# Performance work log

Measured on AMD Instinct MI355X. Metric: run time of the kernel, lower is better.

The kernel has to match this reference:

```python
import jax, jax.numpy as jnp
import numpy as np

D_MODEL, WIN, STRIDE, NHEAD, HEAD_DIM, FFN_H = 96, 16, 8, 6, 16, 192
INNER = NHEAD * HEAD_DIM
EPS = 1e-5


def _ln(x, g, b):
    m = jnp.mean(x, axis=-1, keepdims=True)
    v = jnp.mean((x - m) ** 2, axis=-1, keepdims=True)
    return (x - m) / jnp.sqrt(v + EPS) * g + b


def setup_inputs() -> dict:
    key = jax.random.key(0)
    ks = jax.random.split(key, 16)
    B, L, D = 32, 8192, D_MODEL
    sd = lambda n: 1.0 / np.sqrt(n)
    return {
        "x": jax.random.normal(ks[0], (B, L, D), jnp.float32),
        "ln1_g": jnp.ones((D,), jnp.float32),
        "ln1_b": jnp.zeros((D,), jnp.float32),
        "qkv_w": jax.random.normal(ks[1], (D, 3 * INNER), jnp.float32) * sd(D),
        "qkv_b": jnp.zeros((3 * INNER,), jnp.float32),
        "out_w": jax.random.normal(ks[2], (INNER, D), jnp.float32) * sd(INNER),
        "out_b": jnp.zeros((D,), jnp.float32),
        "ln2_g": jnp.ones((D,), jnp.float32),
        "ln2_b": jnp.zeros((D,), jnp.float32),
        "ffn_w1": jax.random.normal(ks[3], (D, FFN_H), jnp.float32) * sd(D),
        "ffn_b1": jnp.zeros((FFN_H,), jnp.float32),
        "ffn_w2": jax.random.normal(ks[4], (FFN_H, D), jnp.float32) * sd(FFN_H),
        "ffn_b2": jnp.zeros((D,), jnp.float32),
        "pln_g": jnp.ones((D,), jnp.float32),
        "pln_b": jnp.zeros((D,), jnp.float32),
    }


def reference(x, ln1_g, ln1_b, qkv_w, qkv_b, out_w, out_b,
              ln2_g, ln2_b, ffn_w1, ffn_b1, ffn_w2, ffn_b2, pln_g, pln_b):
    B, L, D = x.shape
    w, s = WIN, STRIDE
    num_win = 1 + (L - w) // s  # all windows fit since (num_win-1)*s + w <= L
    idx = jnp.arange(num_win)[:, None] * s + jnp.arange(w)[None, :]  # [N, w]

    seg = x[:, idx]  # [B, N, w, D] gather of overlapping windows

    # --- pre-LN attention block, vectorized over all windows ---
    h = _ln(seg, ln1_g, ln1_b)
    qkv = h @ qkv_w + qkv_b  # [B, N, w, 3*INNER]
    q, k, v = jnp.split(qkv, 3, axis=-1)
    shp = (B, num_win, w, NHEAD, HEAD_DIM)
    q, k, v = q.reshape(shp), k.reshape(shp), v.reshape(shp)
    scores = jnp.einsum('bnqhd,bnkhd->bnhqk', q, k) / np.sqrt(HEAD_DIM).astype(np.float32)
    causal = jnp.tril(jnp.ones((w, w), bool))
    scores = jnp.where(causal, scores, -jnp.inf)
    attn = jax.nn.softmax(scores, axis=-1)
    o = jnp.einsum('bnhqk,bnkhd->bnqhd', attn, v).reshape(B, num_win, w, INNER)
    o = o @ out_w + out_b
    h = seg + o

    # --- FFN block ---
    h2 = _ln(h, ln2_g, ln2_b)
    h = h + (jax.nn.gelu(h2 @ ffn_w1 + ffn_b1) @ ffn_w2 + ffn_b2)
    h = _ln(h, pln_g, pln_b)

    # --- overlap-add average ---
    out = jnp.zeros((B, L, D), x.dtype).at[:, idx].add(h)
    cnt = jnp.zeros((L,), x.dtype).at[idx.reshape(-1)].add(1.0)
    return out / jnp.maximum(cnt, 1.0)[None, :, None]
```

## Files before the change

### kernel.cpp

```cpp
#include <hip/hip_runtime.h>
#include <hip/hip_bf16.h>

typedef __attribute__((ext_vector_type(8))) short short8;
typedef __attribute__((ext_vector_type(4))) float f32x4;

#define LDS_BYTES 40960

#if __has_builtin(__builtin_amdgcn_cvt_pk_bf16_f32)
typedef __attribute__((ext_vector_type(2))) __bf16 bf16x2;
__device__ __forceinline__ unsigned pk2bf(float a, float b){
  bf16x2 v = __builtin_amdgcn_cvt_pk_bf16_f32(a, b);
  return __builtin_bit_cast(unsigned, v);
}
__device__ __forceinline__ unsigned short f2bf(float x){
  bf16x2 v = __builtin_amdgcn_cvt_pk_bf16_f32(x, x);
  return (unsigned short)(__builtin_bit_cast(unsigned, v) & 0xFFFFu);
}
#else
__device__ __forceinline__ unsigned short f2bf(float x){
  unsigned u = __float_as_uint(x);
  u += 0x7FFFu + ((u >> 16) & 1u);
  return (unsigned short)(u >> 16);
}
__device__ __forceinline__ unsigned pk2bf(float a, float b){
  return (unsigned)f2bf(a) | ((unsigned)f2bf(b) << 16);
}
#endif

__device__ __forceinline__ float bflo(unsigned u){ return __uint_as_float(u << 16); }
__device__ __forceinline__ float bfhi(unsigned u){ return __uint_as_float(u & 0xFFFF0000u); }
__device__ __forceinline__ float bf1(unsigned short h){ return __uint_as_float(((unsigned)h) << 16); }

__global__ void zero_stripes(float* __restrict__ out){
  int k = blockIdx.x;
  int b = blockIdx.y;
  int t = threadIdx.x;
  int tok = 24*k + (t / 24);
  f32x4 z = {0.f, 0.f, 0.f, 0.f};
  *(f32x4*)(out + ((size_t)b*8192 + tok)*96 + 4*(t % 24)) = z;
}

__global__ void pack_weights(const float* __restrict__ qkv_w, const float* __restrict__ out_w,
                             const float* __restrict__ ffn_w1, const float* __restrict__ ffn_w2,
                             short8* __restrict__ wsv){
  int f = blockIdx.x, lane = threadIdx.x;
  const float* W; int N, nt, kf;
  if (f < 54)      { W = qkv_w;  N = 288; nt = f/3;        kf = f%3; }
  else if (f < 72) { int i=f-54;  W = out_w;  N = 96;  nt = i/3; kf = i%3; }
  else if (f < 108){ int i=f-72;  W = ffn_w1; N = 192; nt = i/3; kf = i%3; }
  else             { int i=f-108; W = ffn_w2; N = 96;  nt = i/6; kf = i%6; }
  int n = lane & 15, kq = lane >> 4;
  short8 v;
#pragma unroll
  for (int j = 0; j < 8; ++j){
    int k = kf*32 + kq*8 + j;
    v[j] = (short)f2bf(W[(size_t)k * N + nt*16 + n]);
  }
  wsv[f*64 + lane] = v;
}

__global__ __launch_bounds__(512, 8)
void fused_block(const float* __restrict__ x,
                 const float* __restrict__ ln1_g, const float* __restrict__ ln1_b,
                 const float* __restrict__ qkv_b,
                 const float* __restrict__ out_b,
                 const float* __restrict__ ln2_g, const float* __restrict__ ln2_b,
                 const float* __restrict__ ffn_b1, const float* __restrict__ ffn_b2,
                 const float* __restrict__ pln_g, const float* __restrict__ pln_b,
                 const short8* __restrict__ wsv,
                 float* __restrict__ out)
{
  __shared__ __align__(16) char smem[LDS_BYTES];
  unsigned short* hres  = (unsigned short*)smem;
  unsigned*       hresU = (unsigned*)smem;
  unsigned short* Pb    = (unsigned short*)smem;
  unsigned short* buf1  = (unsigned short*)(smem + 9984);
  unsigned*       buf1U = (unsigned*)(smem + 9984);
  unsigned short* buf2  = (unsigned short*)(smem + 19968);
  unsigned*       buf2U = (unsigned*)(smem + 19968);

  const int tid  = threadIdx.x;
  const int wave = tid >> 6, lane = tid & 63;
  const int lm   = lane & 15, quad = lane >> 4;
  const int g = blockIdx.x, b = blockIdx.y;
  const int t0 = 24 * g;
  const size_t xbase = ((size_t)b * 8192 + t0) * 96;

  const int KOFF = 3328;
  const int VOFF = 6656;

  {
    const int row = tid >> 4, j = tid & 15;
    const float* xr = x + xbase + (size_t)row*96 + 6*j;
    float v[6];
#pragma unroll
    for (int e = 0; e < 3; ++e){ float2 t = *(const float2*)(xr + 2*e); v[2*e]=t.x; v[2*e+1]=t.y; }
    float s = 0.f, q2 = 0.f;
#pragma unroll
    for (int e = 0; e < 6; ++e){ s += v[e]; q2 += v[e]*v[e]; }
#pragma unroll
    for (int m = 1; m < 16; m <<= 1){ s += __shfl_xor(s, m, 16); q2 += __shfl_xor(q2, m, 16); }
    float mean = s * (1.f/96.f);
    float rstd = rsqrtf(q2 * (1.f/96.f) - mean*mean + 1e-5f);
#pragma unroll
    for (int e = 0; e < 3; ++e){
      float2 gg = *(const float2*)(ln1_g + 6*j + 2*e);
      float2 bb = *(const float2*)(ln1_b + 6*j + 2*e);
      buf1U[row*52 + 3*j + e] = pk2bf((v[2*e]-mean)*rstd*gg.x+bb.x,
                                      (v[2*e+1]-mean)*rstd*gg.y+bb.y);
    }
  }
  __syncthreads();

  {
    const int mt = wave & 1, p = wave >> 1;
    const unsigned short* arow = buf1 + (16*mt + lm)*104 + quad*8;
    short8 a0 = *(const short8*)(arow);
    short8 a1 = *(const short8*)(arow + 32);
    short8 a2 = *(const short8*)(arow + 64);
    for (int nt = p; nt < 18; nt += 4){
      f32x4 acc = {0.f,0.f,0.f,0.f};
      acc = __builtin_amdgcn_mfma_f32_16x16x32_bf16(a0, wsv[(nt*3+0)*64 + lane], acc, 0, 0, 0);
      acc = __builtin_amdgcn_mfma_f32_16x16x32_bf16(a1, wsv[(nt*3+1)*64 + lane], acc, 0, 0, 0);
      acc = __builtin_amdgcn_mfma_f32_16x16x32_bf16(a2, wsv[(nt*3+2)*64 + lane], acc, 0, 0, 0);
      int col = nt*16 + lm;
      float bias = qkv_b[col];
      if (nt < 6){
#pragma unroll
        for (int r = 0; r < 4; ++r)
          buf2[(16*mt + quad*4 + r)*104 + col] = f2bf(acc[r] + bias);
      } else if (nt < 12){
        int cl = col - 96;
#pragma unroll
        for (int r = 0; r < 4; ++r)
          buf2[KOFF + (16*mt + quad*4 + r)*104 + cl] = f2bf(acc[r] + bias);
      } else {
        int d2 = col - 192;
        int w0 = (VOFF >> 1) + d2*20 + 8*mt + 2*quad;
        buf2U[w0]     = pk2bf(acc[0] + bias, acc[1] + bias);
        buf2U[w0 + 1] = pk2bf(acc[2] + bias, acc[3] + bias);
      }
    }
  }
  __syncthreads();

  for (int u = wave; u < 18; u += 8){
    int w = u / 6, h = u % 6;
    short8 qa = {0,0,0,0,0,0,0,0}, ka = {0,0,0,0,0,0,0,0};
    if (quad < 2){
      qa = *(const short8*)(buf2 +        (8*w + lm)*104 + h*16 + quad*8);
      ka = *(const short8*)(buf2 + KOFF + (8*w + lm)*104 + h*16 + quad*8);
    }
    f32x4 sc = {0.f,0.f,0.f,0.f};
    sc = __builtin_amdgcn_mfma_f32_16x16x32_bf16(qa, ka, sc, 0, 0, 0);
#pragma unroll
    for (int r = 0; r < 4; ++r){
      int row = quad*4 + r;
      float s = (lm <= row) ? sc[r]*0.25f : -1e30f;
      float mx = s;
#pragma unroll
      for (int m = 1; m < 16; m <<= 1) mx = fmaxf(mx, __shfl_xor(mx, m, 16));
      float p = __expf(s - mx);
      float sum = p;
#pragma unroll
      for (int m = 1; m < 16; m <<= 1) sum += __shfl_xor(sum, m, 16);
      Pb[wave*384 + row*24 + lm] = f2bf(p / sum);
    }
    asm volatile("s_waitcnt lgkmcnt(0)" ::: "memory");
    short8 pa = {0,0,0,0,0,0,0,0}, va = {0,0,0,0,0,0,0,0};
    if (quad < 2){
      pa = *(const short8*)(Pb + wave*384 + lm*24 + quad*8);
      va = *(const short8*)(buf2 + VOFF + (h*16 + lm)*40 + 8*w + quad*8);
    }
    f32x4 oc = {0.f,0.f,0.f,0.f};
    oc = __builtin_amdgcn_mfma_f32_16x16x32_bf16(pa, va, oc, 0, 0, 0);
#pragma unroll
    for (int r = 0; r < 4; ++r)
      buf1[(w*16 + quad*4 + r)*104 + h*16 + lm] = f2bf(oc[r]);
  }
  __syncthreads();

  for (int tile = wave; tile < 18; tile += 8){
    int w = tile / 6, nt = tile % 6;
    f32x4 acc = {0.f,0.f,0.f,0.f};
#pragma unroll
    for (int kf = 0; kf < 3; ++kf){
      short8 a = *(const short8*)(buf1 + (w*16 + lm)*104 + kf*32 + quad*8);
      acc = __builtin_amdgcn_mfma_f32_16x16x32_bf16(a, wsv[(54 + nt*3 + kf)*64 + lane], acc, 0, 0, 0);
    }
    int col = nt*16 + lm;
    float bias = out_b[col];
#pragma unroll
    for (int r = 0; r < 4; ++r){
      int i2 = quad*4 + r;
      float seg = x[xbase + (size_t)(8*w + i2)*96 + col];
      hres[(w*16 + i2)*104 + col] = f2bf(acc[r] + bias + seg);
    }
  }
  __syncthreads();

  {
    const int j = tid & 15;
#pragma unroll
    for (int p = 0; p < 2; ++p){
      int row = p*32 + (tid >> 4);
      if (row < 48){
        float v[6];
#pragma unroll
        for (int e = 0; e < 3; ++e){
          unsigned u = hresU[row*52 + 3*j + e];
          v[2*e] = bflo(u); v[2*e+1] = bfhi(u);
        }
        float s = 0.f, q2 = 0.f;
#pragma unroll
        for (int e = 0; e < 6; ++e){ s += v[e]; q2 += v[e]*v[e]; }
#pragma unroll
        for (int m = 1; m < 16; m <<= 1){ s += __shfl_xor(s, m, 16); q2 += __shfl_xor(q2, m, 16); }
        float mean = s * (1.f/96.f);
        float rstd = rsqrtf(q2 * (1.f/96.f) - mean*mean + 1e-5f);
#pragma unroll
        for (int e = 0; e < 3; ++e){
          float2 gg = *(const float2*)(ln2_g + 6*j + 2*e);
          float2 bb = *(const float2*)(ln2_b + 6*j + 2*e);
          buf1U[row*52 + 3*j + e] = pk2bf((v[2*e]-mean)*rstd*gg.x+bb.x,
                                          (v[2*e+1]-mean)*rstd*gg.y+bb.y);
        }
      }
    }
  }
  __syncthreads();

  for (int tile = wave; tile < 36; tile += 8){
    int mt = tile % 3, nt = tile / 3;
    f32x4 acc = {0.f,0.f,0.f,0.f};
#pragma unroll
    for (int kf = 0; kf < 3; ++kf){
      short8 a = *(const short8*)(buf1 + (mt*16 + lm)*104 + kf*32 + quad*8);
      acc = __builtin_amdgcn_mfma_f32_16x16x32_bf16(a, wsv[(72 + nt*3 + kf)*64 + lane], acc, 0, 0, 0);
    }
    float bias = ffn_b1[nt*16 + lm];
#pragma unroll
    for (int r = 0; r < 4; ++r){
      float u = acc[r] + bias;
      float z = 0.7978845608f * (u + 0.044715f * u*u*u);
      z = fminf(fmaxf(z, -10.f), 10.f);
      float e2 = __expf(2.f * z);
      float th = (e2 - 1.f) / (e2 + 1.f);
      buf2[(mt*16 + quad*4 + r)*200 + nt*16 + lm] = f2bf(0.5f * u * (1.f + th));
    }
  }
  __syncthreads();

  for (int tile = wave; tile < 18; tile += 8){
    int mt = tile / 6, nt = tile % 6;
    f32x4 acc = {0.f,0.f,0.f,0.f};
#pragma unroll
    for (int kf = 0; kf < 6; ++kf){
      short8 a = *(const short8*)(buf2 + (mt*16 + lm)*200 + kf*32 + quad*8);
      acc = __builtin_amdgcn_mfma_f32_16x16x32_bf16(a, wsv[(108 + nt*6 + kf)*64 + lane], acc, 0, 0, 0);
    }
    int col = nt*16 + lm;
    float bias = ffn_b2[col];
#pragma unroll
    for (int r = 0; r < 4; ++r){
      int idx = (mt*16 + quad*4 + r)*104 + col;
      hres[idx] = f2bf(bf1(hres[idx]) + acc[r] + bias);
    }
  }
  __syncthreads();

  {
    const int i = tid >> 4, c0 = tid & 15;
    const int l = t0 + i;
    const size_t obase = ((size_t)b * 8192 + l) * 96;
    int rowA, rowB = -1;
    if (i < 8)       rowA = i;
    else if (i < 16){ rowA = i;            rowB = 16 + (i - 8); }
    else if (i < 24){ rowA = 16 + (i - 8); rowB = 32 + (i - 16); }
    else             rowA = 32 + (i - 16);

    float g6[6], b6[6];
#pragma unroll
    for (int e = 0; e < 6; ++e){ g6[e] = pln_g[c0 + 16*e]; b6[e] = pln_b[c0 + 16*e]; }

    float yA[6];
    {
      float v[6];
#pragma unroll
      for (int e = 0; e < 6; ++e) v[e] = bf1(hres[rowA*104 + c0 + 16*e]);
      float s = 0.f, q2 = 0.f;
#pragma unroll
      for (int e = 0; e < 6; ++e){ s += v[e]; q2 += v[e]*v[e]; }
#pragma unroll
      for (int m = 1; m < 16; m <<= 1){ s += __shfl_xor(s, m, 16); q2 += __shfl_xor(q2, m, 16); }
      float mean = s * (1.f/96.f);
      float rstd = rsqrtf(q2 * (1.f/96.f) - mean*mean + 1e-5f);
#pragma unroll
      for (int e = 0; e < 6; ++e) yA[e] = (v[e]-mean)*rstd*g6[e] + b6[e];
    }
    if (rowB >= 0){
      float yB[6];
      {
        float v[6];
#pragma unroll
        for (int e = 0; e < 6; ++e) v[e] = bf1(hres[rowB*104 + c0 + 16*e]);
        float s = 0.f, q2 = 0.f;
#pragma unroll
        for (int e = 0; e < 6; ++e){ s += v[e]; q2 += v[e]*v[e]; }
#pragma unroll
        for (int m = 1; m < 16; m <<= 1){ s += __shfl_xor(s, m, 16); q2 += __shfl_xor(q2, m, 16); }
        float mean = s * (1.f/96.f);
        float rstd = rsqrtf(q2 * (1.f/96.f) - mean*mean + 1e-5f);
#pragma unroll
        for (int e = 0; e < 6; ++e) yB[e] = (v[e]-mean)*rstd*g6[e] + b6[e];
      }
#pragma unroll
      for (int e = 0; e < 6; ++e)
        out[obase + c0 + 16*e] = 0.5f * (yA[e] + yB[e]);
    } else {
      float inv = (l < 8 || l >= 8184) ? 1.0f : 0.5f;
#pragma unroll
      for (int e = 0; e < 6; ++e)
        atomicAdd(&out[obase + c0 + 16*e], yA[e] * inv);
    }
  }
}

extern "C" void kernel_launch(void* const* d_in, const int* in_sizes, int n_in,
                              void* d_out, int out_size, void* d_ws, size_t ws_size,
                              hipStream_t stream) {
  const float* x      = (const float*)d_in[0];
  const float* ln1_g  = (const float*)d_in[1];
  const float* ln1_b  = (const float*)d_in[2];
  const float* qkv_w  = (const float*)d_in[3];
  const float* qkv_b  = (const float*)d_in[4];
  const float* out_w  = (const float*)d_in[5];
  const float* out_b  = (const float*)d_in[6];
  const float* ln2_g  = (const float*)d_in[7];
  const float* ln2_b  = (const float*)d_in[8];
  const float* ffn_w1 = (const float*)d_in[9];
  const float* ffn_b1 = (const float*)d_in[10];
  const float* ffn_w2 = (const float*)d_in[11];
  const float* ffn_b2 = (const float*)d_in[12];
  const float* pln_g  = (const float*)d_in[13];
  const float* pln_b  = (const float*)d_in[14];
  float* out = (float*)d_out;
  short8* wsv = (short8*)d_ws;

  zero_stripes<<<dim3(342, 32), 192, 0, stream>>>(out);
  pack_weights<<<144, 64, 0, stream>>>(qkv_w, out_w, ffn_w1, ffn_w2, wsv);
  fused_block<<<dim3(341, 32), 512, 0, stream>>>(
      x, ln1_g, ln1_b, qkv_b, out_b, ln2_g, ln2_b, ffn_b1, ffn_b2,
      pln_g, pln_b, (const short8*)wsv, out);
}
```

Baseline: 455.8 us.

## Swap MFMA operand order to produce packed row-major outputs and simplify softmax/GELU

Swaps the A/B operands of several MFMAs so each lane holds four consecutive output columns of one row. Results can then be stored as two packed bf16x2 words, with vector bias and residual loads, instead of four scalar bf16 stores. The transposed score layout lets the softmax reduce over four registers plus two cross-quad shuffles instead of eight 16-lane shuffles per row. It also rewrites GELU as u*sigmoid with a hardware reciprocal, and uses hardware rcp/rsq builtins, which trades a little precision for fewer instructions.

Measured after the change: 418.0 us. -8.3%, faster.

```diff
diff --git a/kernel.cpp b/kernel.cpp
--- a/kernel.cpp
+++ b/kernel.cpp
@@ -25,6 +25,17 @@
 __device__ __forceinline__ unsigned pk2bf(float a, float b){
   return (unsigned)f2bf(a) | ((unsigned)f2bf(b) << 16);
 }
+#endif
+
+#if __has_builtin(__builtin_amdgcn_rcpf)
+__device__ __forceinline__ float fast_rcp(float x){ return __builtin_amdgcn_rcpf(x); }
+#else
+__device__ __forceinline__ float fast_rcp(float x){ return 1.f/x; }
+#endif
+#if __has_builtin(__builtin_amdgcn_rsqf)
+__device__ __forceinline__ float fast_rsq(float x){ return __builtin_amdgcn_rsqf(x); }
+#else
+__device__ __forceinline__ float fast_rsq(float x){ return rsqrtf(x); }
 #endif
 
 __device__ __forceinline__ float bflo(unsigned u){ return __uint_as_float(u << 16); }
@@ -74,6 +85,7 @@
   unsigned short* hres  = (unsigned short*)smem;
   unsigned*       hresU = (unsigned*)smem;
   unsigned short* Pb    = (unsigned short*)smem;
+  unsigned*       PbU   = (unsigned*)smem;
   unsigned short* buf1  = (unsigned short*)(smem + 9984);
   unsigned*       buf1U = (unsigned*)(smem + 9984);
   unsigned short* buf2  = (unsigned short*)(smem + 19968);
@@ -101,7 +113,7 @@
 #pragma unroll
     for (int m = 1; m < 16; m <<= 1){ s += __shfl_xor(s, m, 16); q2 += __shfl_xor(q2, m, 16); }
     float mean = s * (1.f/96.f);
-    float rstd = rsqrtf(q2 * (1.f/96.f) - mean*mean + 1e-5f);
+    float rstd = fast_rsq(q2 * (1.f/96.f) - mean*mean + 1e-5f);
 #pragma unroll
     for (int e = 0; e < 3; ++e){
       float2 gg = *(const float2*)(ln1_g + 6*j + 2*e);
@@ -115,26 +127,28 @@
   {
     const int mt = wave & 1, p = wave >> 1;
     const unsigned short* arow = buf1 + (16*mt + lm)*104 + quad*8;
-    short8 a0 = *(const short8*)(arow);
-    short8 a1 = *(const short8*)(arow + 32);
-    short8 a2 = *(const short8*)(arow + 64);
+    short8 h0 = *(const short8*)(arow);
+    short8 h1 = *(const short8*)(arow + 32);
+    short8 h2 = *(const short8*)(arow + 64);
     for (int nt = p; nt < 18; nt += 4){
       f32x4 acc = {0.f,0.f,0.f,0.f};
-      acc = __builtin_amdgcn_mfma_f32_16x16x32_bf16(a0, wsv[(nt*3+0)*64 + lane], acc, 0, 0, 0);
-      acc = __builtin_amdgcn_mfma_f32_16x16x32_bf16(a1, wsv[(nt*3+1)*64 + lane], acc, 0, 0, 0);
-      acc = __builtin_amdgcn_mfma_f32_16x16x32_bf16(a2, wsv[(nt*3+2)*64 + lane], acc, 0, 0, 0);
-      int col = nt*16 + lm;
-      float bias = qkv_b[col];
-      if (nt < 6){
-#pragma unroll
-        for (int r = 0; r < 4; ++r)
-          buf2[(16*mt + quad*4 + r)*104 + col] = f2bf(acc[r] + bias);
-      } else if (nt < 12){
-        int cl = col - 96;
-#pragma unroll
-        for (int r = 0; r < 4; ++r)
-          buf2[KOFF + (16*mt + quad*4 + r)*104 + cl] = f2bf(acc[r] + bias);
+      if (nt < 12){
+        acc = __builtin_amdgcn_mfma_f32_16x16x32_bf16(wsv[(nt*3+0)*64 + lane], h0, acc, 0, 0, 0);
+        acc = __builtin_amdgcn_mfma_f32_16x16x32_bf16(wsv[(nt*3+1)*64 + lane], h1, acc, 0, 0, 0);
+        acc = __builtin_amdgcn_mfma_f32_16x16x32_bf16(wsv[(nt*3+2)*64 + lane], h2, acc, 0, 0, 0);
+        f32x4 b4 = *(const f32x4*)(qkv_b + nt*16 + quad*4);
+        int row = 16*mt + lm;
+        unsigned idx = (nt < 6)
+          ? (unsigned)(row*52 + nt*8 + quad*2)
+          : (unsigned)((KOFF>>1) + row*52 + (nt-6)*8 + quad*2);
+        buf2U[idx]     = pk2bf(acc[0]+b4[0], acc[1]+b4[1]);
+        buf2U[idx + 1] = pk2bf(acc[2]+b4[2], acc[3]+b4[3]);
       } else {
+        acc = __builtin_amdgcn_mfma_f32_16x16x32_bf16(h0, wsv[(nt*3+0)*64 + lane], acc, 0, 0, 0);
+        acc = __builtin_amdgcn_mfma_f32_16x16x32_bf16(h1, wsv[(nt*3+1)*64 + lane], acc, 0, 0, 0);
+        acc = __builtin_amdgcn_mfma_f32_16x16x32_bf16(h2, wsv[(nt*3+2)*64 + lane], acc, 0, 0, 0);
+        int col = nt*16 + lm;
+        float bias = qkv_b[col];
         int d2 = col - 192;
         int w0 = (VOFF >> 1) + d2*20 + 8*mt + 2*quad;
         buf2U[w0]     = pk2bf(acc[0] + bias, acc[1] + bias);
@@ -145,27 +159,32 @@
   __syncthreads();
 
   for (int u = wave; u < 18; u += 8){
-    int w = u / 6, h = u % 6;
+    int w = u / 6, h = u - 6*(u / 6);
     short8 qa = {0,0,0,0,0,0,0,0}, ka = {0,0,0,0,0,0,0,0};
     if (quad < 2){
       qa = *(const short8*)(buf2 +        (8*w + lm)*104 + h*16 + quad*8);
       ka = *(const short8*)(buf2 + KOFF + (8*w + lm)*104 + h*16 + quad*8);
     }
     f32x4 sc = {0.f,0.f,0.f,0.f};
-    sc = __builtin_amdgcn_mfma_f32_16x16x32_bf16(qa, ka, sc, 0, 0, 0);
+    sc = __builtin_amdgcn_mfma_f32_16x16x32_bf16(ka, qa, sc, 0, 0, 0);
+    float s4[4];
 #pragma unroll
     for (int r = 0; r < 4; ++r){
-      int row = quad*4 + r;
-      float s = (lm <= row) ? sc[r]*0.25f : -1e30f;
-      float mx = s;
-#pragma unroll
-      for (int m = 1; m < 16; m <<= 1) mx = fmaxf(mx, __shfl_xor(mx, m, 16));
-      float p = __expf(s - mx);
-      float sum = p;
-#pragma unroll
-      for (int m = 1; m < 16; m <<= 1) sum += __shfl_xor(sum, m, 16);
-      Pb[wave*384 + row*24 + lm] = f2bf(p / sum);
-    }
+      int k = quad*4 + r;
+      s4[r] = (k <= lm) ? sc[r]*0.25f : -1e30f;
+    }
+    float mx = fmaxf(fmaxf(s4[0], s4[1]), fmaxf(s4[2], s4[3]));
+    mx = fmaxf(mx, __shfl_xor(mx, 16));
+    mx = fmaxf(mx, __shfl_xor(mx, 32));
+    float p4[4]; float sum = 0.f;
+#pragma unroll
+    for (int r = 0; r < 4; ++r){ p4[r] = __expf(s4[r] - mx); sum += p4[r]; }
+    sum += __shfl_xor(sum, 16);
+    sum += __shfl_xor(sum, 32);
+    float rs = fast_rcp(sum);
+    unsigned pb = wave*192 + lm*12 + quad*2;
+    PbU[pb]     = pk2bf(p4[0]*rs, p4[1]*rs);
+    PbU[pb + 1] = pk2bf(p4[2]*rs, p4[3]*rs);
     asm volatile("s_waitcnt lgkmcnt(0)" ::: "memory");
     short8 pa = {0,0,0,0,0,0,0,0}, va = {0,0,0,0,0,0,0,0};
     if (quad < 2){
@@ -173,29 +192,26 @@
       va = *(const short8*)(buf2 + VOFF + (h*16 + lm)*40 + 8*w + quad*8);
     }
     f32x4 oc = {0.f,0.f,0.f,0.f};
-    oc = __builtin_amdgcn_mfma_f32_16x16x32_bf16(pa, va, oc, 0, 0, 0);
-#pragma unroll
-    for (int r = 0; r < 4; ++r)
-      buf1[(w*16 + quad*4 + r)*104 + h*16 + lm] = f2bf(oc[r]);
+    oc = __builtin_amdgcn_mfma_f32_16x16x32_bf16(va, pa, oc, 0, 0, 0);
+    unsigned ob = (w*16 + lm)*52 + h*8 + quad*2;
+    buf1U[ob]     = pk2bf(oc[0], oc[1]);
+    buf1U[ob + 1] = pk2bf(oc[2], oc[3]);
   }
   __syncthreads();
 
   for (int tile = wave; tile < 18; tile += 8){
-    int w = tile / 6, nt = tile % 6;
+    int w = tile / 6, nt = tile - 6*(tile / 6);
     f32x4 acc = {0.f,0.f,0.f,0.f};
 #pragma unroll
     for (int kf = 0; kf < 3; ++kf){
-      short8 a = *(const short8*)(buf1 + (w*16 + lm)*104 + kf*32 + quad*8);
-      acc = __builtin_amdgcn_mfma_f32_16x16x32_bf16(a, wsv[(54 + nt*3 + kf)*64 + lane], acc, 0, 0, 0);
-    }
-    int col = nt*16 + lm;
-    float bias = out_b[col];
-#pragma unroll
-    for (int r = 0; r < 4; ++r){
-      int i2 = quad*4 + r;
-      float seg = x[xbase + (size_t)(8*w + i2)*96 + col];
-      hres[(w*16 + i2)*104 + col] = f2bf(acc[r] + bias + seg);
-    }
+      short8 bfr = *(const short8*)(buf1 + (w*16 + lm)*104 + kf*32 + quad*8);
+      acc = __builtin_amdgcn_mfma_f32_16x16x32_bf16(wsv[(54 + nt*3 + kf)*64 + lane], bfr, acc, 0, 0, 0);
+    }
+    f32x4 b4 = *(const f32x4*)(out_b + nt*16 + quad*4);
+    f32x4 xr = *(const f32x4*)(x + xbase + (size_t)(8*w + lm)*96 + nt*16 + quad*4);
+    unsigned idx = (w*16 + lm)*52 + nt*8 + quad*2;
+    hresU[idx]     = pk2bf(acc[0]+b4[0]+xr[0], acc[1]+b4[1]+xr[1]);
+    hresU[idx + 1] = pk2bf(acc[2]+b4[2]+xr[2], acc[3]+b4[3]+xr[3]);
   }
   __syncthreads();
 
@@ -217,7 +233,7 @@
 #pragma unroll
         for (int m = 1; m < 16; m <<= 1){ s += __shfl_xor(s, m, 16); q2 += __shfl_xor(q2, m, 16); }
         float mean = s * (1.f/96.f);
-        float rstd = rsqrtf(q2 * (1.f/96.f) - mean*mean + 1e-5f);
+        float rstd = fast_rsq(q2 * (1.f/96.f) - mean*mean + 1e-5f);
 #pragma unroll
         for (int e = 0; e < 3; ++e){
           float2 gg = *(const float2*)(ln2_g + 6*j + 2*e);
@@ -235,37 +251,37 @@
     f32x4 acc = {0.f,0.f,0.f,0.f};
 #pragma unroll
     for (int kf = 0; kf < 3; ++kf){
-      short8 a = *(const short8*)(buf1 + (mt*16 + lm)*104 + kf*32 + quad*8);
-      acc = __builtin_amdgcn_mfma_f32_16x16x32_bf16(a, wsv[(72 + nt*3 + kf)*64 + lane], acc, 0, 0, 0);
-    }
-    float bias = ffn_b1[nt*16 + lm];
+      short8 bfr = *(const short8*)(buf1 + (mt*16 + lm)*104 + kf*32 + quad*8);
+      acc = __builtin_amdgcn_mfma_f32_16x16x32_bf16(wsv[(72 + nt*3 + kf)*64 + lane], bfr, acc, 0, 0, 0);
+    }
+    f32x4 b4 = *(const f32x4*)(ffn_b1 + nt*16 + quad*4);
+    float gl[4];
 #pragma unroll
     for (int r = 0; r < 4; ++r){
-      float u = acc[r] + bias;
-      float z = 0.7978845608f * (u + 0.044715f * u*u*u);
-      z = fminf(fmaxf(z, -10.f), 10.f);
-      float e2 = __expf(2.f * z);
-      float th = (e2 - 1.f) / (e2 + 1.f);
-      buf2[(mt*16 + quad*4 + r)*200 + nt*16 + lm] = f2bf(0.5f * u * (1.f + th));
-    }
+      float uu = acc[r] + b4[r];
+      float z2n = -1.5957691216f * (uu + 0.044715f * uu*uu*uu);
+      float e = __expf(z2n);
+      gl[r] = uu * fast_rcp(1.f + e);
+    }
+    unsigned idx = (mt*16 + lm)*100 + nt*8 + quad*2;
+    buf2U[idx]     = pk2bf(gl[0], gl[1]);
+    buf2U[idx + 1] = pk2bf(gl[2], gl[3]);
   }
   __syncthreads();
 
   for (int tile = wave; tile < 18; tile += 8){
-    int mt = tile / 6, nt = tile % 6;
+    int mt = tile / 6, nt = tile - 6*(tile / 6);
     f32x4 acc = {0.f,0.f,0.f,0.f};
 #pragma unroll
     for (int kf = 0; kf < 6; ++kf){
-      short8 a = *(const short8*)(buf2 + (mt*16 + lm)*200 + kf*32 + quad*8);
-      acc = __builtin_amdgcn_mfma_f32_16x16x32_bf16(a, wsv[(108 + nt*6 + kf)*64 + lane], acc, 0, 0, 0);
-    }
-    int col = nt*16 + lm;
-    float bias = ffn_b2[col];
-#pragma unroll
-    for (int r = 0; r < 4; ++r){
-      int idx = (mt*16 + quad*4 + r)*104 + col;
-      hres[idx] = f2bf(bf1(hres[idx]) + acc[r] + bias);
-    }
+      short8 bfr = *(const short8*)(buf2 + (mt*16 + lm)*200 + kf*32 + quad*8);
+      acc = __builtin_amdgcn_mfma_f32_16x16x32_bf16(wsv[(108 + nt*6 + kf)*64 + lane], bfr, acc, 0, 0, 0);
+    }
+    f32x4 b4 = *(const f32x4*)(ffn_b2 + nt*16 + quad*4);
+    unsigned idx = (mt*16 + lm)*52 + nt*8 + quad*2;
+    unsigned u0 = hresU[idx], u1 = hresU[idx + 1];
+    hresU[idx]     = pk2bf(bflo(u0)+acc[0]+b4[0], bfhi(u0)+acc[1]+b4[1]);
+    hresU[idx + 1] = pk2bf(bflo(u1)+acc[2]+b4[2], bfhi(u1)+acc[3]+b4[3]);
   }
   __syncthreads();
 
@@ -294,7 +310,7 @@
 #pragma unroll
       for (int m = 1; m < 16; m <<= 1){ s += __shfl_xor(s, m, 16); q2 += __shfl_xor(q2, m, 16); }
       float mean = s * (1.f/96.f);
-      float rstd = rsqrtf(q2 * (1.f/96.f) - mean*mean + 1e-5f);
+      float rstd = fast_rsq(q2 * (1.f/96.f) - mean*mean + 1e-5f);
 #pragma unroll
       for (int e = 0; e < 6; ++e) yA[e] = (v[e]-mean)*rstd*g6[e] + b6[e];
     }
@@ -310,7 +326,7 @@
 #pragma unroll
         for (int m = 1; m < 16; m <<= 1){ s += __shfl_xor(s, m, 16); q2 += __shfl_xor(q2, m, 16); }
         float mean = s * (1.f/96.f);
-        float rstd = rsqrtf(q2 * (1.f/96.f) - mean*mean + 1e-5f);
+        float rstd = fast_rsq(q2 * (1.f/96.f) - mean*mean + 1e-5f);
 #pragma unroll
         for (int e = 0; e < 6; ++e) yB[e] = (v[e]-mean)*rstd*g6[e] + b6[e];
       }
```
